# Performance work log

Measured on AMD Instinct MI355X. Metric: run time of the kernel, lower is better.

## Reference

```python
import jax, jax.numpy as jnp
import numpy as np

N = 100000
E = 1200000
D = 64  # g_dim == h2_dim, heads=1


def setup_inputs() -> dict:
    key = jax.random.key(0)
    ks = jax.random.split(key, 12)
    s = 1.0 / np.sqrt(D)
    node_features = jax.random.normal(ks[0], (N, D), dtype=jnp.float32)
    edge_index = jax.random.randint(ks[1], (2, E), 0, N, dtype=jnp.int64)
    edge_type = jax.random.randint(ks[2], (E,), 0, 4, dtype=jnp.int64)
    Wq = jax.random.uniform(ks[3], (D, D), jnp.float32, -s, s)
    bq = jax.random.uniform(ks[4], (D,), jnp.float32, -s, s)
    Wk = jax.random.uniform(ks[5], (D, D), jnp.float32, -s, s)
    bk = jax.random.uniform(ks[6], (D,), jnp.float32, -s, s)
    Wv = jax.random.uniform(ks[7], (D, D), jnp.float32, -s, s)
    bv = jax.random.uniform(ks[8], (D,), jnp.float32, -s, s)
    Wskip = jax.random.uniform(ks[9], (D, D), jnp.float32, -s, s)
    bskip = jax.random.uniform(ks[10], (D,), jnp.float32, -s, s)
    return dict(node_features=node_features, edge_index=edge_index,
                edge_type=edge_type, Wq=Wq, bq=bq, Wk=Wk, bk=bk,
                Wv=Wv, bv=bv, Wskip=Wskip, bskip=bskip)


def _transformer_conv(x, edge_index, Wq, bq, Wk, bk, Wv, bv, Wskip, bskip):
    src, dst = edge_index[0], edge_index[1]
    q = x @ Wq + bq          # [N, D] queries (for targets)
    k = x @ Wk + bk          # [N, D] keys (for sources)
    v = x @ Wv + bv          # [N, D] values (for sources)
    scale = 1.0 / jnp.sqrt(jnp.asarray(D, x.dtype))
    # per-edge attention logits: (q_dst . k_src) / sqrt(D)   [E]
    logits = jnp.sum(q[dst] * k[src], axis=-1) * scale
    # segment softmax over incoming edges of each destination node
    seg_max = jax.ops.segment_max(logits, dst, num_segments=N)
    seg_max = jnp.where(jnp.isfinite(seg_max), seg_max, 0.0)
    ex = jnp.exp(logits - seg_max[dst])
    seg_sum = jax.ops.segment_sum(ex, dst, num_segments=N)
    alpha = ex / (seg_sum[dst] + 1e-16)                      # [E]
    # attention-weighted scatter-aggregate of source values
    out = jax.ops.segment_sum(alpha[:, None] * v[src], dst, num_segments=N)
    # root/skip connection
    return out + x @ Wskip + bskip


def reference(node_features, edge_index, edge_type, Wq, bq, Wk, bk, Wv, bv, Wskip, bskip):
    # edge_type is accepted but unused, matching the original forward.
    return _transformer_conv(node_features, edge_index, Wq, bq, Wk, bk, Wv, bv, Wskip, bskip)
```

## Files before the change

### kernel.cpp

```cpp
#include <hip/hip_runtime.h>
#include <hip/hip_fp16.h>

#define D 64
#define BSH 9
#define SPLIT_CH 4096
#define NH 512
#define QSCALE 0.18033688f

typedef _Float16 f16x2 __attribute__((ext_vector_type(2)));
typedef _Float16 f16x8 __attribute__((ext_vector_type(8)));
typedef float f32x4 __attribute__((ext_vector_type(4)));

__device__ __forceinline__ float fdot2f(f16x2 a, f16x2 b, float c) {
#if __has_builtin(__builtin_amdgcn_fdot2)
    return __builtin_amdgcn_fdot2(a, b, c, false);
#else
    return fmaf((float)a.x, (float)b.x, fmaf((float)a.y, (float)b.y, c));
#endif
}

__device__ __forceinline__ f16x2 shxor_h2(f16x2 v, int m) {
    int i = __builtin_bit_cast(int, v);
    i = __shfl_xor(i, m);
    return __builtin_bit_cast(f16x2, i);
}

__device__ __forceinline__ unsigned packh2(float a, float b) {
    __half2 h = __floats2half2_rn(a, b);
    return __builtin_bit_cast(unsigned, h);
}

__global__ __launch_bounds__(256) void k_prep(
    const float* __restrict__ Wq, const float* __restrict__ Wk,
    const float* __restrict__ Wv, const float* __restrict__ Wsk,
    const float* __restrict__ bq, const float* __restrict__ bk,
    const float* __restrict__ bv, const float* __restrict__ bsk,
    unsigned* __restrict__ wpk, float* __restrict__ ball,
    int* __restrict__ ghist, int* __restrict__ gcur0)
{
    const int t = threadIdx.x;
    if (blockIdx.x < 32) {
        const int u    = blockIdx.x * 256 + t;
        const int i2   = u & 3;
        const int lane = (u >> 2) & 63;
        const int ks   = (u >> 8) & 1;
        const int mt   = u >> 9;
        const int ncol = mt * 16 + (lane & 15);
        const int k0   = ks * 32 + ((lane >> 4) << 3) + (i2 << 1);
        const float* W; int c; float sc = 1.f;
        if      (ncol <  64) { W = Wq;  c = ncol;       sc = QSCALE; }
        else if (ncol < 128) { W = Wk;  c = ncol - 64;  }
        else if (ncol < 192) { W = Wv;  c = ncol - 128; }
        else                 { W = Wsk; c = ncol - 192; }
        wpk[u] = packh2(W[k0 * 64 + c] * sc, W[(k0 + 1) * 64 + c] * sc);
    } else {
        ghist[t] = 0;
        gcur0[t] = 0;
        float b;
        if      (t <  64) b = bq[t] * QSCALE;
        else if (t < 128) b = bk[t - 64];
        else if (t < 192) b = bv[t - 128];
        else              b = bsk[t - 192];
        ball[t] = b;
    }
}

__global__ __launch_bounds__(256) void k_histlin(
    const float* __restrict__ x, const unsigned* __restrict__ wpk,
    const float* __restrict__ ball,
    const int* __restrict__ ei, int* __restrict__ ghist,
    unsigned* __restrict__ qh, unsigned* __restrict__ kvh,
    float* __restrict__ out, int n, int e_cnt, int NLIN)
{
    __shared__ __align__(16) _Float16 xsh[16][72];
    const int t = threadIdx.x;

    if (blockIdx.x >= NLIN) {
        int* h = (int*)xsh;
        h[t] = 0;
        __syncthreads();
        const int hb    = blockIdx.x - NLIN;
        const int chunk = (e_cnt + NH - 1) / NH;
        const int c0    = hb * chunk;
        const int c1    = min(c0 + chunk, e_cnt);
        for (int i = c0 + t; i < c1; i += 256)
            atomicAdd(&h[ei[e_cnt + i] >> BSH], 1);
        __syncthreads();
        if (h[t]) atomicAdd(&ghist[t], h[t]);
        return;
    }

    const int node0 = blockIdx.x * 16;
    {
        const float4* xg = (const float4*)(x + (size_t)node0 * 64);
        const int row = t >> 4, c4 = (t & 15) << 2;
        if (node0 + row < n) {
            const float4 v = xg[t];
            f16x2* dst = (f16x2*)&xsh[row][c4];
            dst[0] = f16x2{(_Float16)v.x, (_Float16)v.y};
            dst[1] = f16x2{(_Float16)v.z, (_Float16)v.w};
        }
    }
    __syncthreads();

    const int w  = t >> 6;
    const int l  = t & 63;
    const int nd = l & 15;
    const int kg = l >> 4;

    f32x4 acc0 = {0.f, 0.f, 0.f, 0.f};
    f32x4 acc1 = acc0, acc2 = acc0, acc3 = acc0;
    const uint4* wpk4 = (const uint4*)wpk;

#pragma unroll
    for (int ks = 0; ks < 2; ++ks) {
        const f16x8 bfrag = *(const f16x8*)&xsh[nd][ks * 32 + kg * 8];
        const int fb = (w * 4 * 2 + ks) * 64 + l;
        const f16x8 a0 = __builtin_bit_cast(f16x8, wpk4[fb]);
        const f16x8 a1 = __builtin_bit_cast(f16x8, wpk4[fb + 128]);
        const f16x8 a2 = __builtin_bit_cast(f16x8, wpk4[fb + 256]);
        const f16x8 a3 = __builtin_bit_cast(f16x8, wpk4[fb + 384]);
        acc0 = __builtin_amdgcn_mfma_f32_16x16x32_f16(a0, bfrag, acc0, 0, 0, 0);
        acc1 = __builtin_amdgcn_mfma_f32_16x16x32_f16(a1, bfrag, acc1, 0, 0, 0);
        acc2 = __builtin_amdgcn_mfma_f32_16x16x32_f16(a2, bfrag, acc2, 0, 0, 0);
        acc3 = __builtin_amdgcn_mfma_f32_16x16x32_f16(a3, bfrag, acc3, 0, 0, 0);
    }

    const int node = node0 + nd;
    if (node >= n) return;

    f32x4 accs[4] = {acc0, acc1, acc2, acc3};
#pragma unroll
    for (int m4 = 0; m4 < 4; ++m4) {
        const int gc = (w * 4 + m4) * 16 + kg * 4;
        const float4 bb = ((const float4*)ball)[gc >> 2];
        const float v0 = accs[m4][0] + bb.x;
        const float v1 = accs[m4][1] + bb.y;
        const float v2 = accs[m4][2] + bb.z;
        const float v3 = accs[m4][3] + bb.w;
        if (w == 3) {
            ((float4*)out)[(size_t)node * 16 + ((gc - 192) >> 2)] =
                make_float4(v0, v1, v2, v3);
        } else {
            uint2 u;
            u.x = packh2(v0, v1);
            u.y = packh2(v2, v3);
            if (w == 0)
                ((uint2*)qh)[(size_t)node * 16 + (gc >> 2)] = u;
            else if (w == 1)
                ((uint2*)kvh)[(size_t)node * 32 + ((gc - 64) >> 2)] = u;
            else
                ((uint2*)kvh)[(size_t)node * 32 + 16 + ((gc - 128) >> 2)] = u;
        }
    }
}

__global__ __launch_bounds__(256) void k_split(
    const int* __restrict__ ei, const int* __restrict__ ghist,
    int* __restrict__ gcur0, unsigned* __restrict__ epack, int e_cnt)
{
    __shared__ unsigned vals[SPLIT_CH];
    __shared__ int addr[SPLIT_CH];
    __shared__ int hist[256], start[256], cur[256], base[256], s2[256], sg[256];

    const int t  = threadIdx.x;
    const int e0 = blockIdx.x * SPLIT_CH;
    const int cnt = min(SPLIT_CH, e_cnt - e0);

    hist[t] = 0;
    __syncthreads();
    for (int i = t; i < cnt; i += 256)
        atomicAdd(&hist[ei[e_cnt + e0 + i] >> BSH], 1);
    __syncthreads();

    {
        const int v = hist[t];
        const int g = ghist[t];
        s2[t] = v;
        sg[t] = g;
        __syncthreads();
        for (int off = 1; off < 256; off <<= 1) {
            const int a1 = (t >= off) ? s2[t - off] : 0;
            const int a2 = (t >= off) ? sg[t - off] : 0;
            __syncthreads();
            s2[t] += a1;
            sg[t] += a2;
            __syncthreads();
        }
        start[t] = s2[t] - v;
        cur[t]   = s2[t] - v;
        base[t]  = v ? (sg[t] - g + atomicAdd(&gcur0[t], v)) : 0;
    }
    __syncthreads();

    for (int i = t; i < cnt; i += 256) {
        const int s = ei[e0 + i];
        const int d = ei[e_cnt + e0 + i];
        const int b = d >> BSH;
        const int r = atomicAdd(&cur[b], 1);
        vals[r] = ((unsigned)s << BSH) | (unsigned)(d & 511);
        addr[r] = base[b] + (r - start[b]);
    }
    __syncthreads();

    for (int i = t; i < cnt; i += 256)
        epack[addr[i]] = vals[i];
}

__global__ __launch_bounds__(512) void k_nodesort(
    const unsigned* __restrict__ epack, const int* __restrict__ ghist,
    int* __restrict__ esrc, int* __restrict__ endoff, int n)
{
    __shared__ int h[512], cur[512], s[512];
    __shared__ int sbase;
    const int b = blockIdx.x;
    const int t = threadIdx.x;

    s[t] = (t < 256) ? ghist[t] : 0;
    __syncthreads();
    for (int off = 1; off < 512; off <<= 1) {
        const int add = (t >= off) ? s[t - off] : 0;
        __syncthreads();
        s[t] += add;
        __syncthreads();
    }
    if (t == 0) sbase = (b == 0) ? 0 : s[b - 1];
    __syncthreads();
    const int base = sbase;
    const int cnt  = ghist[b];

    h[t] = 0;
    __syncthreads();
    for (int i = t; i < cnt; i += 512)
        atomicAdd(&h[epack[base + i] & 511], 1);
    __syncthreads();

    const int v = h[t];
    s[t] = v;
    __syncthreads();
    for (int off = 1; off < 512; off <<= 1) {
        const int add = (t >= off) ? s[t - off] : 0;
        __syncthreads();
        s[t] += add;
        __syncthreads();
    }
    cur[t] = s[t] - v;
    const int node = (b << BSH) + t;
    if (node < n) endoff[node] = base + s[t];
    __syncthreads();

    for (int i = t; i < cnt; i += 512) {
        const unsigned p = epack[base + i];
        const int r = atomicAdd(&cur[p & 511], 1);
        esrc[base + r] = (int)(p >> BSH);
    }
}

__global__ __launch_bounds__(256) void k_attn(
    const uint4* __restrict__ qh4, const uint4* __restrict__ kv4,
    const int* __restrict__ endoff, const int* __restrict__ esrc,
    float* __restrict__ out, int n)
{
    const int t = threadIdx.x;
    const int node = blockIdx.x * 4 + (t >> 6);
    if (node >= n) return;
    const int lane = t & 63;
    const int g = lane >> 3;
    const int l = lane & 7;

    const int beg = (node == 0) ? 0 : endoff[node - 1];
    const int end = endoff[node];
    const int last = end - 1;

    float4 o0 = make_float4(0.f, 0.f, 0.f, 0.f);
    float4 o1 = o0;
    if (g == 0) {
        o0 = ((const float4*)out)[(size_t)node * 16 + 2 * l];
        o1 = ((const float4*)out)[(size_t)node * 16 + 2 * l + 1];
    }

    const uint4 qu = qh4[(size_t)node * 8 + l];
    const f16x2* qp = (const f16x2*)&qu;

    f16x2 a0 = {(_Float16)0.f, (_Float16)0.f};
    f16x2 a1 = a0, a2 = a0, a3 = a0;
    float den = 0.f;

    int b2 = beg;
    for (; end - b2 > 8; b2 += 16) {
        const int iA = b2 + 2 * g;
        const int iB = iA + 1;
        const int sA = esrc[min(iA, last)];
        const int sB = esrc[min(iB, last)];
        const uint4 kuA = kv4[(size_t)sA * 16 + l];
        const uint4 vuA = kv4[(size_t)sA * 16 + 8 + l];
        const uint4 kuB = kv4[(size_t)sB * 16 + l];
        const uint4 vuB = kv4[(size_t)sB * 16 + 8 + l];
        const f16x2* kpA = (const f16x2*)&kuA;
        const f16x2* vpA = (const f16x2*)&vuA;
        const f16x2* kpB = (const f16x2*)&kuB;
        const f16x2* vpB = (const f16x2*)&vuB;

        float dA = fdot2f(qp[0], kpA[0], 0.f);
        float dB = fdot2f(qp[0], kpB[0], 0.f);
        dA = fdot2f(qp[1], kpA[1], dA);
        dB = fdot2f(qp[1], kpB[1], dB);
        dA = fdot2f(qp[2], kpA[2], dA);
        dB = fdot2f(qp[2], kpB[2], dB);
        dA = fdot2f(qp[3], kpA[3], dA);
        dB = fdot2f(qp[3], kpB[3], dB);
        dA += __shfl_xor(dA, 1);  dB += __shfl_xor(dB, 1);
        dA += __shfl_xor(dA, 2);  dB += __shfl_xor(dB, 2);
        dA += __shfl_xor(dA, 4);  dB += __shfl_xor(dB, 4);

        const float eA = (iA < end) ? exp2f(dA) : 0.f;
        const float eB = (iB < end) ? exp2f(dB) : 0.f;
        den += eA + eB;
        const _Float16 ehA = (_Float16)eA;
        const _Float16 ehB = (_Float16)eB;
        const f16x2 e2A = {ehA, ehA};
        const f16x2 e2B = {ehB, ehB};
        a0 += e2A * vpA[0];  a0 += e2B * vpB[0];
        a1 += e2A * vpA[1];  a1 += e2B * vpB[1];
        a2 += e2A * vpA[2];  a2 += e2B * vpB[2];
        a3 += e2A * vpA[3];  a3 += e2B * vpB[3];
    }
    for (; b2 < end; b2 += 8) {
        const int i = b2 + g;
        const int s = esrc[min(i, last)];
        const uint4 ku = kv4[(size_t)s * 16 + l];
        const uint4 vu = kv4[(size_t)s * 16 + 8 + l];
        const f16x2* kp = (const f16x2*)&ku;
        const f16x2* vp = (const f16x2*)&vu;

        float d = fdot2f(qp[0], kp[0], 0.f);
        d = fdot2f(qp[1], kp[1], d);
        d = fdot2f(qp[2], kp[2], d);
        d = fdot2f(qp[3], kp[3], d);
        d += __shfl_xor(d, 1);
        d += __shfl_xor(d, 2);
        d += __shfl_xor(d, 4);

        const float e = (i < end) ? exp2f(d) : 0.f;
        den += e;
        const _Float16 eh = (_Float16)e;
        const f16x2 e2 = {eh, eh};
        a0 += e2 * vp[0];
        a1 += e2 * vp[1];
        a2 += e2 * vp[2];
        a3 += e2 * vp[3];
    }

#pragma unroll
    for (int m = 8; m <= 32; m <<= 1) {
        den += __shfl_xor(den, m);
        a0 += shxor_h2(a0, m);
        a1 += shxor_h2(a1, m);
        a2 += shxor_h2(a2, m);
        a3 += shxor_h2(a3, m);
    }

    if (g == 0) {
        const float inv = 1.f / (den + 1e-16f);
        float4 r0, r1;
        r0.x = o0.x + (float)a0.x * inv;
        r0.y = o0.y + (float)a0.y * inv;
        r0.z = o0.z + (float)a1.x * inv;
        r0.w = o0.w + (float)a1.y * inv;
        r1.x = o1.x + (float)a2.x * inv;
        r1.y = o1.y + (float)a2.y * inv;
        r1.z = o1.z + (float)a3.x * inv;
        r1.w = o1.w + (float)a3.y * inv;
        ((float4*)out)[(size_t)node * 16 + 2 * l]     = r0;
        ((float4*)out)[(size_t)node * 16 + 2 * l + 1] = r1;
    }
}

extern "C" void kernel_launch(void* const* d_in, const int* in_sizes, int n_in,
                              void* d_out, int out_size, void* d_ws, size_t ws_size,
                              hipStream_t stream)
{
    const float* x   = (const float*)d_in[0];
    const int*   ei  = (const int*)d_in[1];
    const float* Wq  = (const float*)d_in[3];
    const float* bq  = (const float*)d_in[4];
    const float* Wk  = (const float*)d_in[5];
    const float* bk  = (const float*)d_in[6];
    const float* Wv  = (const float*)d_in[7];
    const float* bv  = (const float*)d_in[8];
    const float* Wsk = (const float*)d_in[9];
    const float* bsk = (const float*)d_in[10];
    float* out = (float*)d_out;

    const int n     = in_sizes[0] / D;
    const int e_cnt = in_sizes[1] / 2;
    const int nbkt  = (n + 511) >> BSH;
    const int NLIN  = (n + 15) / 16;

    unsigned* qh     = (unsigned*)d_ws;
    unsigned* kvh    = qh + (size_t)n * 32;
    int*      esrc   = (int*)(kvh + (size_t)n * 64);
    unsigned* epack  = (unsigned*)(esrc + e_cnt);
    int*      endoff = (int*)(epack + e_cnt);
    int*      ghist  = endoff + n;
    int*      gcur0  = ghist + 256;
    float*    ball   = (float*)(gcur0 + 256);
    unsigned* wpk    = (unsigned*)(ball + 256);

    k_prep<<<33, 256, 0, stream>>>(
        Wq, Wk, Wv, Wsk, bq, bk, bv, bsk, wpk, ball, ghist, gcur0);

    k_histlin<<<NLIN + NH, 256, 0, stream>>>(
        x, wpk, ball, ei, ghist, qh, kvh, out, n, e_cnt, NLIN);

    k_split<<<(e_cnt + SPLIT_CH - 1) / SPLIT_CH, 256, 0, stream>>>(
        ei, ghist, gcur0, epack, e_cnt);

    k_nodesort<<<nbkt, 512, 0, stream>>>(
        epack, ghist, esrc, endoff, n);

    k_attn<<<(n + 3) / 4, 256, 0, stream>>>(
        (const uint4*)qh, (const uint4*)kvh, endoff, esrc, out, n);
}
```

Before: 124.2 us.

## Move histogram into prep kernel and fuse linear projection with bucket split

The global destination-bucket histogram moves into the weight-prep kernel, so the split pass no longer waits on the linear projection. The split pass is then merged into the same launch as the projection, so their blocks can run concurrently. Zeroing of the counters moves to a memset. The split blocks now keep a one-byte bucket id per edge in shared memory instead of a full address array, which shrinks their shared-memory footprint. The cost is that projection blocks are sized to the larger union of shared memory, which may lower their occupancy.

```diff
diff --git a/kernel.cpp b/kernel.cpp
--- a/kernel.cpp
+++ b/kernel.cpp
@@ -35,8 +35,8 @@
     const float* __restrict__ Wv, const float* __restrict__ Wsk,
     const float* __restrict__ bq, const float* __restrict__ bk,
     const float* __restrict__ bv, const float* __restrict__ bsk,
-    unsigned* __restrict__ wpk, float* __restrict__ ball,
-    int* __restrict__ ghist, int* __restrict__ gcur0)
+    const int* __restrict__ ei, unsigned* __restrict__ wpk,
+    float* __restrict__ ball, int* __restrict__ ghist, int e_cnt)
 {
     const int t = threadIdx.x;
     if (blockIdx.x < 32) {
@@ -53,33 +53,18 @@
         else if (ncol < 192) { W = Wv;  c = ncol - 128; }
         else                 { W = Wsk; c = ncol - 192; }
         wpk[u] = packh2(W[k0 * 64 + c] * sc, W[(k0 + 1) * 64 + c] * sc);
-    } else {
-        ghist[t] = 0;
-        gcur0[t] = 0;
+    } else if (blockIdx.x == 32) {
         float b;
         if      (t <  64) b = bq[t] * QSCALE;
         else if (t < 128) b = bk[t - 64];
         else if (t < 192) b = bv[t - 128];
         else              b = bsk[t - 192];
         ball[t] = b;
-    }
-}
-
-__global__ __launch_bounds__(256) void k_histlin(
-    const float* __restrict__ x, const unsigned* __restrict__ wpk,
-    const float* __restrict__ ball,
-    const int* __restrict__ ei, int* __restrict__ ghist,
-    unsigned* __restrict__ qh, unsigned* __restrict__ kvh,
-    float* __restrict__ out, int n, int e_cnt, int NLIN)
-{
-    __shared__ __align__(16) _Float16 xsh[16][72];
-    const int t = threadIdx.x;
-
-    if (blockIdx.x >= NLIN) {
-        int* h = (int*)xsh;
+    } else {
+        __shared__ int h[256];
         h[t] = 0;
         __syncthreads();
-        const int hb    = blockIdx.x - NLIN;
+        const int hb    = blockIdx.x - 33;
         const int chunk = (e_cnt + NH - 1) / NH;
         const int c0    = hb * chunk;
         const int c1    = min(c0 + chunk, e_cnt);
@@ -87,6 +72,80 @@
             atomicAdd(&h[ei[e_cnt + i] >> BSH], 1);
         __syncthreads();
         if (h[t]) atomicAdd(&ghist[t], h[t]);
+    }
+}
+
+__global__ __launch_bounds__(256) void k_linsplit(
+    const float* __restrict__ x, const unsigned* __restrict__ wpk,
+    const float* __restrict__ ball, const int* __restrict__ ei,
+    const int* __restrict__ ghist, int* __restrict__ gcur0,
+    unsigned* __restrict__ qh, unsigned* __restrict__ kvh,
+    float* __restrict__ out, unsigned* __restrict__ epack,
+    int n, int e_cnt, int NLIN)
+{
+    __shared__ __align__(16) union {
+        struct {
+            unsigned vals[SPLIT_CH];
+            unsigned char bkt[SPLIT_CH];
+            int hist[256], start[256], cur[256], base[256], s2[256], sg[256];
+        } sp;
+        _Float16 xsh[16][72];
+    } sm;
+    const int t = threadIdx.x;
+
+    if (blockIdx.x >= NLIN) {
+        unsigned* vals = sm.sp.vals;
+        unsigned char* bkt = sm.sp.bkt;
+        int* hist  = sm.sp.hist;
+        int* start = sm.sp.start;
+        int* cur   = sm.sp.cur;
+        int* base  = sm.sp.base;
+        int* s2    = sm.sp.s2;
+        int* sg    = sm.sp.sg;
+
+        const int e0  = (blockIdx.x - NLIN) * SPLIT_CH;
+        const int cnt = min(SPLIT_CH, e_cnt - e0);
+
+        hist[t] = 0;
+        __syncthreads();
+        for (int i = t; i < cnt; i += 256)
+            atomicAdd(&hist[ei[e_cnt + e0 + i] >> BSH], 1);
+        __syncthreads();
+
+        {
+            const int v = hist[t];
+            const int g = ghist[t];
+            s2[t] = v;
+            sg[t] = g;
+            __syncthreads();
+            for (int off = 1; off < 256; off <<= 1) {
+                const int a1 = (t >= off) ? s2[t - off] : 0;
+                const int a2 = (t >= off) ? sg[t - off] : 0;
+                __syncthreads();
+                s2[t] += a1;
+                sg[t] += a2;
+                __syncthreads();
+            }
+            start[t] = s2[t] - v;
+            cur[t]   = s2[t] - v;
+            base[t]  = v ? (sg[t] - g + atomicAdd(&gcur0[t], v)) : 0;
+        }
+        __syncthreads();
+
+        for (int i = t; i < cnt; i += 256) {
+            const int s = ei[e0 + i];
+            const int d = ei[e_cnt + e0 + i];
+            const int b = d >> BSH;
+            const int r = atomicAdd(&cur[b], 1);
+            vals[r] = ((unsigned)s << BSH) | (unsigned)(d & 511);
+            bkt[r]  = (unsigned char)b;
+        }
+        __syncthreads();
+
+        for (int i = t; i < cnt; i += 256) {
+            const int b = bkt[i];
+            epack[base[b] + (i - start[b])] = vals[i];
+        }
         return;
     }
 
@@ -96,7 +155,7 @@
         const int row = t >> 4, c4 = (t & 15) << 2;
         if (node0 + row < n) {
             const float4 v = xg[t];
-            f16x2* dst = (f16x2*)&xsh[row][c4];
+            f16x2* dst = (f16x2*)&sm.xsh[row][c4];
             dst[0] = f16x2{(_Float16)v.x, (_Float16)v.y};
             dst[1] = f16x2{(_Float16)v.z, (_Float16)v.w};
         }
@@ -114,7 +173,7 @@
 
 #pragma unroll
     for (int ks = 0; ks < 2; ++ks) {
-        const f16x8 bfrag = *(const f16x8*)&xsh[nd][ks * 32 + kg * 8];
+        const f16x8 bfrag = *(const f16x8*)&sm.xsh[nd][ks * 32 + kg * 8];
         const int fb = (w * 4 * 2 + ks) * 64 + l;
         const f16x8 a0 = __builtin_bit_cast(f16x8, wpk4[fb]);
         const f16x8 a1 = __builtin_bit_cast(f16x8, wpk4[fb + 128]);
@@ -155,58 +214,6 @@
     }
 }
 
-__global__ __launch_bounds__(256) void k_split(
-    const int* __restrict__ ei, const int* __restrict__ ghist,
-    int* __restrict__ gcur0, unsigned* __restrict__ epack, int e_cnt)
-{
-    __shared__ unsigned vals[SPLIT_CH];
-    __shared__ int addr[SPLIT_CH];
-    __shared__ int hist[256], start[256], cur[256], base[256], s2[256], sg[256];
-
-    const int t  = threadIdx.x;
-    const int e0 = blockIdx.x * SPLIT_CH;
-    const int cnt = min(SPLIT_CH, e_cnt - e0);
-
-    hist[t] = 0;
-    __syncthreads();
-    for (int i = t; i < cnt; i += 256)
-        atomicAdd(&hist[ei[e_cnt + e0 + i] >> BSH], 1);
-    __syncthreads();
-
-    {
-        const int v = hist[t];
-        const int g = ghist[t];
-        s2[t] = v;
-        sg[t] = g;
-        __syncthreads();
-        for (int off = 1; off < 256; off <<= 1) {
-            const int a1 = (t >= off) ? s2[t - off] : 0;
-            const int a2 = (t >= off) ? sg[t - off] : 0;
-            __syncthreads();
-            s2[t] += a1;
-            sg[t] += a2;
-            __syncthreads();
-        }
-        start[t] = s2[t] - v;
-        cur[t]   = s2[t] - v;
-        base[t]  = v ? (sg[t] - g + atomicAdd(&gcur0[t], v)) : 0;
-    }
-    __syncthreads();
-
-    for (int i = t; i < cnt; i += 256) {
-        const int s = ei[e0 + i];
-        const int d = ei[e_cnt + e0 + i];
-        const int b = d >> BSH;
-        const int r = atomicAdd(&cur[b], 1);
-        vals[r] = ((unsigned)s << BSH) | (unsigned)(d & 511);
-        addr[r] = base[b] + (r - start[b]);
-    }
-    __syncthreads();
-
-    for (int i = t; i < cnt; i += 256)
-        epack[addr[i]] = vals[i];
-}
-
 __global__ __launch_bounds__(512) void k_nodesort(
     const unsigned* __restrict__ epack, const int* __restrict__ ghist,
     int* __restrict__ esrc, int* __restrict__ endoff, int n)
@@ -392,10 +399,11 @@
     const float* bsk = (const float*)d_in[10];
     float* out = (float*)d_out;
 
-    const int n     = in_sizes[0] / D;
-    const int e_cnt = in_sizes[1] / 2;
-    const int nbkt  = (n + 511) >> BSH;
-    const int NLIN  = (n + 15) / 16;
+    const int n      = in_sizes[0] / D;
+    const int e_cnt  = in_sizes[1] / 2;
+    const int nbkt   = (n + 511) >> BSH;
+    const int NLIN   = (n + 15) / 16;
+    const int NSPLIT = (e_cnt + SPLIT_CH - 1) / SPLIT_CH;
 
     unsigned* qh     = (unsigned*)d_ws;
     unsigned* kvh    = qh + (size_t)n * 32;
@@ -407,14 +415,13 @@
     float*    ball   = (float*)(gcur0 + 256);
     unsigned* wpk    = (unsigned*)(ball + 256);
 
-    k_prep<<<33, 256, 0, stream>>>(
-        Wq, Wk, Wv, Wsk, bq, bk, bv, bsk, wpk, ball, ghist, gcur0);
-
-    k_histlin<<<NLIN + NH, 256, 0, stream>>>(
-        x, wpk, ball, ei, ghist, qh, kvh, out, n, e_cnt, NLIN);
-
-    k_split<<<(e_cnt + SPLIT_CH - 1) / SPLIT_CH, 256, 0, stream>>>(
-        ei, ghist, gcur0, epack, e_cnt);
+    hipMemsetAsync(ghist, 0, 512 * sizeof(int), stream);
+
+    k_prep<<<33 + NH, 256, 0, stream>>>(
+        Wq, Wk, Wv, Wsk, bq, bk, bv, bsk, ei, wpk, ball, ghist, e_cnt);
+
+    k_linsplit<<<NLIN + NSPLIT, 256, 0, stream>>>(
+        x, wpk, ball, ei, ghist, gcur0, qh, kvh, out, epack, n, e_cnt, NLIN);
 
     k_nodesort<<<nbkt, 512, 0, stream>>>(
         epack, ghist, esrc, endoff, n);
```

Measured after the change: 124.1 us (median of 3 runs). Within noise of the previous version (-0.1%).
